# Optimization experiments

Hardware: AMD Instinct MI355X
Metric: run time of the kernel (lower is better)

The kernel has to match this reference:

```python
import jax, jax.numpy as jnp
import numpy as np

N, D, K = 8192, 128, 30  # num_nodes, isize, k


def setup_inputs() -> dict:
    key = jax.random.key(0)
    k1, k2, k3 = jax.random.split(key, 3)
    features = jax.random.normal(k1, (N, D), dtype=jnp.float32)
    # module initializes layers to identity; perturb slightly so weights matter
    eye = jnp.eye(D, dtype=jnp.float32)
    W1 = eye + 0.02 * jax.random.normal(k2, (D, D), dtype=jnp.float32)
    W2 = eye + 0.02 * jax.random.normal(k3, (D, D), dtype=jnp.float32)
    b1 = jnp.zeros((D,), dtype=jnp.float32)
    b2 = jnp.zeros((D,), dtype=jnp.float32)
    return {"features": features, "W1": W1, "b1": b1, "W2": W2, "b2": b2, "kp1": K + 1}


def reference(features, W1, b1, W2, b2, kp1):
    # internal_forward: Linear -> ReLU -> Linear (act='relu', last layer no act)
    h = jax.nn.relu(features @ W1.T + b1)
    emb = h @ W2.T + b2
    # F.normalize(dim=1, p=2)
    emb = emb / jnp.clip(jnp.linalg.norm(emb, axis=1, keepdims=True), 1e-12, None)
    # cal_similarity_graph: dense cosine similarity [N, N]
    sim = emb @ emb.T
    # top_k: keep top (k+1) entries per row, zero the rest
    _, idx = jax.lax.top_k(sim, kp1)  # idx: [N, kp1]
    mask = jnp.zeros_like(sim).at[jnp.arange(sim.shape[0])[:, None], idx].set(1.0)
    sparse_graph = sim * mask
    # apply_non_linearity('relu', i): elementwise relu
    return jax.nn.relu(sparse_graph)
```

## Files before the change

### kernel.cpp

```cpp
#include <hip/hip_runtime.h>
#include <hip/hip_fp16.h>

#define NN 8192
#define DDIM 128
#define DELTA 0.010f
#define MAXC 256
#define SIMSTRIDE 16384

typedef short short8 __attribute__((ext_vector_type(8)));
typedef unsigned short ushort8 __attribute__((ext_vector_type(8)));
typedef float f32x16 __attribute__((ext_vector_type(16)));

__device__ __forceinline__ ushort bf16_rne(float v) {
    const unsigned x = __float_as_uint(v);
    return (ushort)((x + 0x7FFFu + ((x >> 16) & 1u)) >> 16);
}

__global__ __launch_bounds__(128, 1)
void mlp_norm_kernel(const float* __restrict__ X, const float* __restrict__ W1,
                     const float* __restrict__ b1, const float* __restrict__ W2,
                     const float* __restrict__ b2, float* __restrict__ emb,
                     ushort* __restrict__ ebh, int rowsPerBlock)
{
    const int t = threadIdx.x;
    float4 w1r[32], w2r[32];
#pragma unroll
    for (int i = 0; i < 32; ++i) w1r[i] = *(const float4*)&W1[t * DDIM + i * 4];
#pragma unroll
    for (int i = 0; i < 32; ++i) w2r[i] = *(const float4*)&W2[t * DDIM + i * 4];
    const float bb1 = b1[t], bb2 = b2[t];

    __shared__ float sx[DDIM];
    __shared__ float sh[DDIM];
    __shared__ float wred[2];

    const int row0 = blockIdx.x * rowsPerBlock;
    for (int r = 0; r < rowsPerBlock; ++r) {
        const int row = row0 + r;
        sx[t] = X[(size_t)row * DDIM + t];
        __syncthreads();
        float acc = bb1;
#pragma unroll
        for (int i = 0; i < 32; ++i) {
            const float4 xv = *(const float4*)&sx[i * 4];
            acc = fmaf(xv.x, w1r[i].x, acc);
            acc = fmaf(xv.y, w1r[i].y, acc);
            acc = fmaf(xv.z, w1r[i].z, acc);
            acc = fmaf(xv.w, w1r[i].w, acc);
        }
        sh[t] = fmaxf(acc, 0.f);
        __syncthreads();
        float acc2 = bb2;
#pragma unroll
        for (int i = 0; i < 32; ++i) {
            const float4 hv = *(const float4*)&sh[i * 4];
            acc2 = fmaf(hv.x, w2r[i].x, acc2);
            acc2 = fmaf(hv.y, w2r[i].y, acc2);
            acc2 = fmaf(hv.z, w2r[i].z, acc2);
            acc2 = fmaf(hv.w, w2r[i].w, acc2);
        }
        float sq = acc2 * acc2;
#pragma unroll
        for (int off = 1; off < 64; off <<= 1) sq += __shfl_xor(sq, off);
        if ((t & 63) == 0) wred[t >> 6] = sq;
        __syncthreads();
        const float ss = wred[0] + wred[1];
        const float inv = 1.0f / fmaxf(sqrtf(ss), 1e-12f);
        const float v = acc2 * inv;
        emb[(size_t)row * DDIM + t] = v;
        ebh[(size_t)row * DDIM + t] = bf16_rne(v);
        __syncthreads();
    }
}

__global__ __launch_bounds__(256)
void simgemm_bf16(const ushort* __restrict__ ebh, ushort* __restrict__ sim)
{
    __shared__ ushort lA[128 * 128];
    __shared__ ushort lB[128 * 128];

    const int tid = threadIdx.x;
    const int bi = blockIdx.x & 63, bj = blockIdx.x >> 6;
    const int m0 = bi << 7, n0 = bj << 7;
    const int lane = tid & 63, wid = tid >> 6;
    const int wr = wid >> 1, wc = wid & 1;
    const int frow = lane & 31, fsel = lane >> 5;

    const int srow0 = tid >> 4, sg = tid & 15;
#pragma unroll
    for (int i = 0; i < 8; ++i) {
        const int row = srow0 + i * 16;
        const int so = row * 128 + ((sg ^ (row & 15)) << 3);
        *(uint4*)&lA[so] = *(const uint4*)&ebh[(size_t)(m0 + row) * DDIM + sg * 8];
        *(uint4*)&lB[so] = *(const uint4*)&ebh[(size_t)(n0 + row) * DDIM + sg * 8];
    }
    __syncthreads();

    f32x16 acc[2][2];
#pragma unroll
    for (int mb = 0; mb < 2; ++mb)
#pragma unroll
        for (int nb = 0; nb < 2; ++nb)
#pragma unroll
            for (int q = 0; q < 16; ++q) acc[mb][nb][q] = 0.f;

#pragma unroll
    for (int ks = 0; ks < 8; ++ks) {
        const int g = ks * 2 + fsel;
        short8 av[2], bv[2];
#pragma unroll
        for (int mb = 0; mb < 2; ++mb) {
            const int r = wr * 64 + mb * 32 + frow;
            av[mb] = *(const short8*)&lA[r * 128 + ((g ^ (r & 15)) << 3)];
        }
#pragma unroll
        for (int nb = 0; nb < 2; ++nb) {
            const int r = wc * 64 + nb * 32 + frow;
            bv[nb] = *(const short8*)&lB[r * 128 + ((g ^ (r & 15)) << 3)];
        }
#pragma unroll
        for (int mb = 0; mb < 2; ++mb)
#pragma unroll
            for (int nb = 0; nb < 2; ++nb)
                acc[mb][nb] = __builtin_amdgcn_mfma_f32_32x32x16_bf16(
                    av[mb], bv[nb], acc[mb][nb], 0, 0, 0);
    }

    __syncthreads();
#pragma unroll
    for (int mb = 0; mb < 2; ++mb)
#pragma unroll
        for (int nb = 0; nb < 2; ++nb) {
            const int cl = wc * 64 + nb * 32 + (lane & 31);
#pragma unroll
            for (int q = 0; q < 16; ++q) {
                const int rl = wr * 64 + mb * 32 + (q & 3) + 8 * (q >> 2) + 4 * fsel;
                lA[rl * 128 + cl] = __half_as_ushort(__float2half_rn(acc[mb][nb][q]));
            }
        }
    __syncthreads();
    {
        const int rr0 = tid >> 4, cc = (tid & 15) * 8;
#pragma unroll
        for (int i = 0; i < 8; ++i) {
            const int row = rr0 + i * 16;
            *(uint4*)&sim[(size_t)(m0 + row) * SIMSTRIDE + n0 + cc] =
                *(const uint4*)&lA[row * 128 + cc];
        }
    }
}

__global__ __launch_bounds__(256)
void topk_relu_kernel(float* __restrict__ out, const float* __restrict__ emb,
                      const int* __restrict__ kp1p)
{
    const int row = blockIdx.x;
    const int t = threadIdx.x;
    const int w = t >> 6;
    const int lane = t & 63;
    const unsigned kp1 = (unsigned)kp1p[0];
    const ushort* simrow = (const ushort*)out + (size_t)row * SIMSTRIDE;
    float* rowp = out + (size_t)row * NN;

    __shared__ unsigned bitmap[NN / 32];
    __shared__ float semb[DDIM];
    __shared__ unsigned hist[4][256];
    __shared__ unsigned wpart[4];
    __shared__ unsigned sHL[2];
    __shared__ int cidx[MAXC];
    __shared__ float cval[MAXC];
    __shared__ int cnum;

    bitmap[t] = 0;
    hist[0][t] = 0; hist[1][t] = 0; hist[2][t] = 0; hist[3][t] = 0;
    if (t == 0) cnum = 0;
    if (t < DDIM) semb[t] = emb[(size_t)row * DDIM + t];
    __syncthreads();

    unsigned u[32];
#pragma unroll
    for (int i = 0; i < 4; ++i) {
        const ushort8 v8 = *(const ushort8*)&simrow[i * 2048 + t * 8];
#pragma unroll
        for (int j = 0; j < 8; ++j) {
            const unsigned uu = (v8[j] < 0x8000u) ? (unsigned)v8[j] : 0u;
            u[i * 8 + j] = uu;
            if (uu) atomicAdd(&hist[w][uu >> 6], 1u);
        }
    }
    __syncthreads();

    const unsigned tot = hist[0][t] + hist[1][t] + hist[2][t] + hist[3][t];
    unsigned s = tot;
#pragma unroll
    for (int off = 1; off < 64; off <<= 1) {
        const unsigned o = __shfl_down(s, off);
        if (lane + off < 64) s += o;
    }
    if (lane == 0) wpart[w] = s;
    __syncthreads();
    unsigned addhi = 0;
    for (int w2 = w + 1; w2 < 4; ++w2) addhi += wpart[w2];
    const unsigned S = s + addhi;
    if (t == 0 && wpart[0] + wpart[1] + wpart[2] + wpart[3] < kp1) {
        sHL[0] = 0u; sHL[1] = 0xFFFFFFFFu;
    }
    if (S >= kp1 && S - tot < kp1) {
        const unsigned B = (unsigned)t;
        const float L = __half2float(__ushort_as_half((ushort)(B << 6)));
        const float H = __half2float(__ushort_as_half((ushort)((B << 6) | 63u)));
        const unsigned hi =
            (unsigned)__half_as_ushort(__float2half_rn(H + DELTA)) + 1u;
        const float lof = L - DELTA;
        unsigned lo;
        if (lof <= 0.f) lo = 1u;
        else { const unsigned l2 = __half_as_ushort(__float2half_rn(lof));
               lo = (l2 > 1u) ? l2 - 1u : 1u; }
        sHL[0] = hi; sHL[1] = lo;
    }
    __syncthreads();

    const unsigned hi16 = sHL[0], lo16 = sHL[1];
    if (hi16 != 0u) {
        unsigned acnt = 0;
#pragma unroll
        for (int q = 0; q < 32; ++q) {
            const unsigned uu = u[q];
            if (uu > hi16) ++acnt;
            else if (uu >= lo16) {
                const int p = atomicAdd(&cnum, 1);
                if (p < MAXC) cidx[p] = (q >> 3) * 2048 + t * 8 + (q & 7);
            }
        }
#pragma unroll
        for (int off = 1; off < 64; off <<= 1) acnt += __shfl_xor(acnt, off);
        if (lane == 0) wpart[w] = acnt;
        __syncthreads();
        const unsigned A = wpart[0] + wpart[1] + wpart[2] + wpart[3];
        const int nc = cnum < MAXC ? cnum : MAXC;

        if (t < nc) {
            const float* rb = emb + (size_t)cidx[t] * DDIM;
            float a = 0.f;
#pragma unroll 8
            for (int k = 0; k < DDIM; ++k) a = fmaf(semb[k], rb[k], a);
            cval[t] = a;
        }
        __syncthreads();
        if (t < nc) {
            const float e = cval[t];
            const int my = cidx[t];
            int r = 0;
            for (int d = 0; d < nc; ++d)
                r += (cval[d] > e) || (cval[d] == e && cidx[d] < my);
            if (A + (unsigned)r < kp1)
                atomicOr(&bitmap[my >> 5], 1u << (my & 31));
        }
        __syncthreads();
    } else {
        __syncthreads();
    }

#pragma unroll
    for (int i = 0; i < 4; ++i) {
        const int col0 = i * 2048 + t * 8;
        float o[8];
#pragma unroll
        for (int j = 0; j < 8; ++j) {
            const unsigned uu = u[i * 8 + j];
            const int idx = col0 + j;
            const bool keep = (uu > hi16) ||
                              (uu >= lo16 &&
                               ((bitmap[idx >> 5] >> (idx & 31)) & 1u));
            o[j] = keep ? __half2float(__ushort_as_half((ushort)uu)) : 0.f;
        }
        *(float4*)&rowp[col0]     = make_float4(o[0], o[1], o[2], o[3]);
        *(float4*)&rowp[col0 + 4] = make_float4(o[4], o[5], o[6], o[7]);
    }
}

extern "C" void kernel_launch(void* const* d_in, const int* in_sizes, int n_in,
                              void* d_out, int out_size, void* d_ws, size_t ws_size,
                              hipStream_t stream)
{
    const float* X  = (const float*)d_in[0];
    const float* W1 = (const float*)d_in[1];
    const float* b1 = (const float*)d_in[2];
    const float* W2 = (const float*)d_in[3];
    const float* b2 = (const float*)d_in[4];
    const int* kp1  = (const int*)d_in[5];
    float* out = (float*)d_out;
    float* emb  = (float*)d_ws;
    ushort* ebh = (ushort*)((char*)d_ws + (size_t)NN * DDIM * 4);

    mlp_norm_kernel<<<512, 128, 0, stream>>>(X, W1, b1, W2, b2, emb, ebh, 16);
    simgemm_bf16<<<4096, 256, 0, stream>>>(ebh, (ushort*)out);
    topk_relu_kernel<<<NN, 256, 0, stream>>>(out, emb, kp1);
}
```

Before: 221.3 us.

## Store sim tile directly to global and spread histogram over 8 padded copies

The GEMM epilogue now writes each fp16 accumulator element straight to global memory, dropping the LDS staging pass and its two barriers, at the cost of narrow 2-byte strided stores instead of coalesced 16-byte ones. The top-k kernel replaces the per-wave histogram with 8 lane-interleaved copies padded to a stride of 260. This is meant to cut atomic contention on hot bins, with slightly more LDS to clear and to reduce.

```diff
diff --git a/kernel.cpp b/kernel.cpp
--- a/kernel.cpp
+++ b/kernel.cpp
@@ -6,6 +6,8 @@
 #define DELTA 0.010f
 #define MAXC 256
 #define SIMSTRIDE 16384
+#define HC 8
+#define HSTRIDE 260
 
 typedef short short8 __attribute__((ext_vector_type(8)));
 typedef unsigned short ushort8 __attribute__((ext_vector_type(8)));
@@ -126,28 +128,18 @@
                     av[mb], bv[nb], acc[mb][nb], 0, 0, 0);
     }
 
-    __syncthreads();
 #pragma unroll
     for (int mb = 0; mb < 2; ++mb)
 #pragma unroll
-        for (int nb = 0; nb < 2; ++nb) {
-            const int cl = wc * 64 + nb * 32 + (lane & 31);
+        for (int nb = 0; nb < 2; ++nb)
 #pragma unroll
             for (int q = 0; q < 16; ++q) {
-                const int rl = wr * 64 + mb * 32 + (q & 3) + 8 * (q >> 2) + 4 * fsel;
-                lA[rl * 128 + cl] = __half_as_ushort(__float2half_rn(acc[mb][nb][q]));
+                const int rl = (q & 3) + 8 * (q >> 2) + 4 * fsel;
+                const int grow = m0 + wr * 64 + mb * 32 + rl;
+                const int gcol = n0 + wc * 64 + nb * 32 + (lane & 31);
+                sim[(size_t)grow * SIMSTRIDE + gcol] =
+                    __half_as_ushort(__float2half_rn(acc[mb][nb][q]));
             }
-        }
-    __syncthreads();
-    {
-        const int rr0 = tid >> 4, cc = (tid & 15) * 8;
-#pragma unroll
-        for (int i = 0; i < 8; ++i) {
-            const int row = rr0 + i * 16;
-            *(uint4*)&sim[(size_t)(m0 + row) * SIMSTRIDE + n0 + cc] =
-                *(const uint4*)&lA[row * 128 + cc];
-        }
-    }
 }
 
 __global__ __launch_bounds__(256)
@@ -164,7 +156,7 @@
 
     __shared__ unsigned bitmap[NN / 32];
     __shared__ float semb[DDIM];
-    __shared__ unsigned hist[4][256];
+    __shared__ unsigned hist[HC * HSTRIDE];
     __shared__ unsigned wpart[4];
     __shared__ unsigned sHL[2];
     __shared__ int cidx[MAXC];
@@ -172,11 +164,12 @@
     __shared__ int cnum;
 
     bitmap[t] = 0;
-    hist[0][t] = 0; hist[1][t] = 0; hist[2][t] = 0; hist[3][t] = 0;
+    for (int i = t; i < HC * HSTRIDE; i += 256) hist[i] = 0u;
     if (t == 0) cnum = 0;
     if (t < DDIM) semb[t] = emb[(size_t)row * DDIM + t];
     __syncthreads();
 
+    const int hc = (t & 7) * HSTRIDE;
     unsigned u[32];
 #pragma unroll
     for (int i = 0; i < 4; ++i) {
@@ -185,12 +178,14 @@
         for (int j = 0; j < 8; ++j) {
             const unsigned uu = (v8[j] < 0x8000u) ? (unsigned)v8[j] : 0u;
             u[i * 8 + j] = uu;
-            if (uu) atomicAdd(&hist[w][uu >> 6], 1u);
-        }
-    }
-    __syncthreads();
-
-    const unsigned tot = hist[0][t] + hist[1][t] + hist[2][t] + hist[3][t];
+            if (uu) atomicAdd(&hist[hc + (uu >> 6)], 1u);
+        }
+    }
+    __syncthreads();
+
+    unsigned tot = 0;
+#pragma unroll
+    for (int c = 0; c < HC; ++c) tot += hist[c * HSTRIDE + t];
     unsigned s = tot;
 #pragma unroll
     for (int off = 1; off < 64; off <<= 1) {
```

New measurement: 218.4 us. No clear change (-1.3%).
